# Optimization experiments

Hardware: AMD Instinct MI355X
Metric: run time of the kernel (lower is better)

Reference implementation:

```python
import jax, jax.numpy as jnp
import numpy as np

EPS = 1e-12

def l2norm(x, axis):
    # torch.nn.functional.normalize: x / max(||x||_2, eps)
    n = jnp.sqrt(jnp.sum(x * x, axis=axis, keepdims=True))
    return x / jnp.maximum(n, EPS)

def setup_inputs() -> dict:
    key = jax.random.key(0)
    k1, k2, k3, k4 = jax.random.split(key, 4)
    B, Cf, H, W = 128, 1024, 16, 16
    n_att, dv = 312, 300
    img = jax.random.normal(k1, (B, Cf, H, W), dtype=jnp.float32)
    # V is initialized from row-normalized w2v embeddings in the module
    V = l2norm(jax.random.normal(k2, (n_att, dv), dtype=jnp.float32), axis=1)
    W1 = jax.random.normal(k3, (dv, Cf), dtype=jnp.float32)
    W2 = jax.random.normal(k4, (dv, Cf), dtype=jnp.float32)
    return {"img": img, "V": V, "W1": W1, "W2": W2}

def reference(img, V, W1, W2):
    vv = l2norm(V, axis=1)                               # [i, v]
    B, Cf, H, Wd = img.shape
    av = l2norm(img.reshape(B, Cf, H * Wd), axis=1)      # [b, f, r]
    Q = vv @ W1                                          # [i, f]
    A = jnp.einsum('if,bfr->bir', Q, av)                 # attention logits
    A = jax.nn.softmax(A, axis=-1)
    F_p = jnp.einsum('bir,bfr->bif', A, av)              # attended features
    Pred_att = jnp.einsum('if,bif->bi', vv @ W2, F_p)
    return Pred_att
```

## Files before the change

kernel.cpp:

```cpp
#include <hip/hip_runtime.h>
#include <math.h>

#define NB   128
#define CF   1024
#define RR   256
#define NA   312
#define DV   300
#define MT   640
#define NKC  32
#define NQ   160
#define NPI  320
#define ABYTES 40960

typedef _Float16 half8  __attribute__((ext_vector_type(8)));
typedef _Float16 half4  __attribute__((ext_vector_type(4)));
typedef float float16v  __attribute__((ext_vector_type(16)));
typedef float float4v   __attribute__((ext_vector_type(4)));

__device__ __forceinline__ void gll16(const void* g, void* l) {
    __builtin_amdgcn_global_load_lds(
        (const __attribute__((address_space(1))) void*)g,
        (__attribute__((address_space(3))) void*)l, 16, 0, 0);
}

__launch_bounds__(256, 4)
__global__ void k_q(const float* __restrict__ V, const float* __restrict__ W1,
                    const float* __restrict__ W2, _Float16* __restrict__ Qb) {
    int ib = blockIdx.x;
    int t  = threadIdx.x;
    bool isQ2 = ib >= 80;
    int i0l = (ib - (isQ2 ? 80 : 0)) * 4;
    __shared__ float inv4[4];
    float acc[4][4];
    #pragma unroll
    for (int ii = 0; ii < 4; ++ii)
        #pragma unroll
        for (int j = 0; j < 4; ++j) acc[ii][j] = 0.f;
    if (i0l < NA) {
        int row = t >> 6, l64 = t & 63;
        float s = 0.f;
        for (int v = l64; v < DV; v += 64) { float x = V[(i0l + row) * DV + v]; s += x * x; }
        #pragma unroll
        for (int o = 32; o; o >>= 1) s += __shfl_xor(s, o, 64);
        if (l64 == 0) inv4[row] = 1.f / fmaxf(sqrtf(s), 1e-12f);
        __syncthreads();
        const float* W  = isQ2 ? W2 : W1;
        const float* Vb = V + (size_t)i0l * DV;
        for (int v = 0; v < DV; v += 2) {
            float4v w0 = *(const float4v*)(W + (size_t)v * CF + t * 4);
            float4v w1 = *(const float4v*)(W + (size_t)(v + 1) * CF + t * 4);
            #pragma unroll
            for (int ii = 0; ii < 4; ++ii) {
                float a0 = Vb[(size_t)ii * DV + v];
                float a1 = Vb[(size_t)ii * DV + v + 1];
                #pragma unroll
                for (int j = 0; j < 4; ++j) acc[ii][j] += a0 * w0[j] + a1 * w1[j];
            }
        }
        #pragma unroll
        for (int ii = 0; ii < 4; ++ii)
            #pragma unroll
            for (int j = 0; j < 4; ++j) acc[ii][j] *= inv4[ii];
    }
    int fg = t >> 3;
    int fo = (t & 7) * 4;
    int q12 = isQ2 ? 1 : 0;
    #pragma unroll
    for (int ii = 0; ii < 4; ++ii) {
        half4 h;
        #pragma unroll
        for (int j = 0; j < 4; ++j) h[j] = (_Float16)acc[ii][j];
        *(half4*)&Qb[((size_t)fg * MT + (2 * (i0l + ii) + q12)) * 32 + fo] = h;
    }
}

extern __shared__ char smem[];
__launch_bounds__(512, 2)
__global__ void k_fused(const float* __restrict__ img, const _Float16* __restrict__ Qb,
                        float* __restrict__ pm, float* __restrict__ ps,
                        float* __restrict__ pd) {
    int lin = blockIdx.x;
    int b   = lin >> 1;
    int rh  = lin & 1;

    int tid  = threadIdx.x;
    int lane = tid & 63;
    int w    = tid >> 6;
    int wm   = w >> 1;
    int wn   = w & 1;
    int nl   = lane & 31;
    int kh   = lane >> 5;

    int aG[5];
    #pragma unroll
    for (int j = 0; j < 5; ++j) {
        int s = tid + j * 512;
        aG[j] = ((s % 640) * 4 + (s / 640)) * 16;
    }
    const char* gA = (const char*)Qb;

    int c_lo = wn * 64 + nl;
    const float* pB = img + (size_t)b * CF * RR + (size_t)rh * 128 + c_lo
                      + (size_t)kh * 8 * RR;

    float16v acc[5][2];
    #pragma unroll
    for (int i = 0; i < 5; ++i)
        #pragma unroll
        for (int j = 0; j < 2; ++j)
            #pragma unroll
            for (int gi = 0; gi < 16; ++gi) acc[i][j][gi] = 0.f;
    float ssq0 = 0.f, ssq1 = 0.f;
    float Bv0[2][8], Bv1[2][8];
    half8 bf0[2], bf1[2];

    #define AGLL(kc_, bsel) do {                                                   \
        int kcl = (kc_) < NKC ? (kc_) : (NKC - 1);                                 \
        const char* aS = gA + (size_t)kcl * ABYTES;                                \
        char* buf_ = smem + (size_t)(bsel) * ABYTES;                               \
        _Pragma("unroll")                                                          \
        for (int j = 0; j < 5; ++j) gll16(aS + aG[j], buf_ + (tid + j * 512) * 16); \
    } while (0)

    #define BLOAD(kc_) do {                                                        \
        int kcl = (kc_) < NKC ? (kc_) : (NKC - 1);                                 \
        const float* p = pB + (size_t)kcl * 32 * RR;                               \
        _Pragma("unroll")                                                          \
        for (int ks = 0; ks < 2; ++ks)                                             \
            _Pragma("unroll")                                                      \
            for (int j = 0; j < 8; ++j) {                                          \
                Bv0[ks][j] = p[(size_t)(ks * 16 + j) * RR];                        \
                Bv1[ks][j] = p[(size_t)(ks * 16 + j) * RR + 32];                   \
            }                                                                      \
    } while (0)

    #define BCVT() do {                                                            \
        _Pragma("unroll")                                                          \
        for (int ks = 0; ks < 2; ++ks)                                             \
            _Pragma("unroll")                                                      \
            for (int j = 0; j < 8; ++j) {                                          \
                float x0 = Bv0[ks][j], x1 = Bv1[ks][j];                            \
                ssq0 += x0 * x0; ssq1 += x1 * x1;                                  \
                bf0[ks][j] = (_Float16)x0; bf1[ks][j] = (_Float16)x1;              \
            }                                                                      \
    } while (0)

    #define COMPUTE(bsel) do {                                                     \
        const char* Al = smem + (size_t)(bsel) * ABYTES;                           \
        _Pragma("unroll")                                                          \
        for (int ks = 0; ks < 2; ++ks) {                                           \
            int kb = ks * 2 + kh;                                                  \
            _Pragma("unroll")                                                      \
            for (int mt = 0; mt < 5; ++mt) {                                       \
                half8 af = *(const half8*)(Al + ((size_t)kb * 640 + wm * 160 + mt * 32 + nl) * 16); \
                acc[mt][0] = __builtin_amdgcn_mfma_f32_32x32x16_f16(af, bf0[ks], acc[mt][0], 0, 0, 0); \
                acc[mt][1] = __builtin_amdgcn_mfma_f32_32x32x16_f16(af, bf1[ks], acc[mt][1], 0, 0, 0); \
            }                                                                      \
        }                                                                          \
    } while (0)

    AGLL(0, 0);
    BLOAD(0);
    asm volatile("s_waitcnt vmcnt(32)" ::: "memory");
    __builtin_amdgcn_s_barrier();
    AGLL(1, 1);
    __builtin_amdgcn_sched_barrier(0);

    #pragma unroll 1
    for (int kc = 0; kc < NKC; ++kc) {
        asm volatile("s_waitcnt vmcnt(5)" ::: "memory");
        BCVT();
        BLOAD(kc + 1);
        __builtin_amdgcn_sched_barrier(0);
        __builtin_amdgcn_s_setprio(1);
        COMPUTE(kc & 1);
        __builtin_amdgcn_s_setprio(0);
        __builtin_amdgcn_sched_barrier(0);
        asm volatile("s_waitcnt vmcnt(32)" ::: "memory");
        __builtin_amdgcn_s_barrier();
        AGLL(kc + 2, kc & 1);
        __builtin_amdgcn_sched_barrier(0);
    }
    asm volatile("s_waitcnt vmcnt(0) lgkmcnt(0)" ::: "memory");
    __builtin_amdgcn_s_barrier();
    __builtin_amdgcn_sched_barrier(0);
    #undef AGLL
    #undef BLOAD
    #undef BCVT
    #undef COMPUTE

    float* mred = (float*)smem;
    float* mg   = (float*)(smem + 2560);
    float* sred = (float*)(smem + 3840);
    float* dred = (float*)(smem + 6400);

    ssq0 += __shfl_xor(ssq0, 32, 64);
    ssq1 += __shfl_xor(ssq1, 32, 64);
    float iv0 = 1.f / fmaxf(sqrtf(ssq0), 1e-12f);
    float iv1 = 1.f / fmaxf(sqrtf(ssq1), 1e-12f);
    #pragma unroll
    for (int mt = 0; mt < 5; ++mt)
        #pragma unroll
        for (int gi = 0; gi < 16; ++gi) {
            acc[mt][0][gi] *= iv0;
            acc[mt][1][gi] *= iv1;
        }

    #pragma unroll
    for (int mt = 0; mt < 5; ++mt) {
        #pragma unroll
        for (int e = 0; e < 8; ++e) {
            int g = 2 * e;
            float mx = fmaxf(acc[mt][0][g], acc[mt][1][g]);
            #pragma unroll
            for (int off = 1; off <= 16; off <<= 1)
                mx = fmaxf(mx, __shfl_xor(mx, off, 64));
            if (nl == 0) {
                int row = (g & 3) + 8 * (g >> 2) + 4 * kh;
                mred[wn * NPI + wm * 80 + mt * 16 + (row >> 1)] = mx;
            }
        }
    }
    __syncthreads();
    if (tid < NPI) mg[tid] = fmaxf(mred[tid], mred[NPI + tid]);
    __syncthreads();

    #pragma unroll
    for (int mt = 0; mt < 5; ++mt) {
        #pragma unroll
        for (int e = 0; e < 8; ++e) {
            int g = 2 * e;
            int row = (g & 3) + 8 * (g >> 2) + 4 * kh;
            int i   = wm * 80 + mt * 16 + (row >> 1);
            float m  = mg[i];
            float e0 = __expf(acc[mt][0][g] - m);
            float e1 = __expf(acc[mt][1][g] - m);
            float s = e0 + e1;
            float d = e0 * acc[mt][0][g + 1] + e1 * acc[mt][1][g + 1];
            #pragma unroll
            for (int off = 1; off <= 16; off <<= 1) {
                s += __shfl_xor(s, off, 64);
                d += __shfl_xor(d, off, 64);
            }
            if (nl == 0) {
                sred[wn * NPI + i] = s;
                dred[wn * NPI + i] = d;
            }
        }
    }
    __syncthreads();
    if (tid < NPI) {
        size_t pb = ((size_t)b * 2 + rh) * NPI + tid;
        pm[pb] = mg[tid];
        ps[pb] = sred[tid] + sred[NPI + tid];
        pd[pb] = dred[tid] + dred[NPI + tid];
    }
}

__launch_bounds__(256, 4)
__global__ void k_comb(const float* __restrict__ pm, const float* __restrict__ ps,
                       const float* __restrict__ pd, float* __restrict__ out) {
    int idx = blockIdx.x * 256 + threadIdx.x;
    int b = idx / NPI;
    int i = idx - b * NPI;
    float m0 = pm[(size_t)(b * 2) * NPI + i];
    float m1 = pm[(size_t)(b * 2 + 1) * NPI + i];
    float m  = fmaxf(m0, m1);
    float w0 = __expf(m0 - m), w1 = __expf(m1 - m);
    float s = ps[(size_t)(b * 2) * NPI + i] * w0 + ps[(size_t)(b * 2 + 1) * NPI + i] * w1;
    float d = pd[(size_t)(b * 2) * NPI + i] * w0 + pd[(size_t)(b * 2 + 1) * NPI + i] * w1;
    if (i < NA) out[(size_t)b * NA + i] = d / s;
}

extern "C" void kernel_launch(void* const* d_in, const int* in_sizes, int n_in,
                              void* d_out, int out_size, void* d_ws, size_t ws_size,
                              hipStream_t stream) {
    const float* img = (const float*)d_in[0];
    const float* V   = (const float*)d_in[1];
    const float* W1  = (const float*)d_in[2];
    const float* W2  = (const float*)d_in[3];
    float* out = (float*)d_out;

    char* ws = (char*)d_ws;
    size_t off = 0;
    _Float16* Qb = (_Float16*)(ws + off); off += (size_t)NKC * MT * 32 * 2;
    float*    pm = (float*)(ws + off);    off += (size_t)NB * 2 * NPI * 4;
    float*    ps = (float*)(ws + off);    off += (size_t)NB * 2 * NPI * 4;
    float*    pd = (float*)(ws + off);    off += (size_t)NB * 2 * NPI * 4;

    static bool attr_done = false;
    if (!attr_done) {
        (void)hipFuncSetAttribute((const void*)k_fused,
                                  hipFuncAttributeMaxDynamicSharedMemorySize, 2 * ABYTES);
        attr_done = true;
    }

    k_q<<<dim3(NQ), 256, 0, stream>>>(V, W1, W2, Qb);
    k_fused<<<dim3(256), 512, 2 * ABYTES, stream>>>(img, Qb, pm, ps, pd);
    k_comb<<<dim3(160), 256, 0, stream>>>(pm, ps, pd, out);
}
```

Before: 273.4 us.

## Split fused attention kernel across M quarters into smaller 128-thread blocks

The fused kernel now launches 1024 blocks of two waves, each covering one quarter of the attribute rows for a batch/r-half, instead of 256 blocks of eight waves. The Q tile staged in LDS shrinks to that quarter and moves to static shared memory, so the dynamic-LDS attribute setup is dropped. This aims to spread work over more CUs and raise occupancy. In exchange, each image slice is read and converted four times, relying on L2 for reuse.

After: 278.1 us. Within noise of the previous version (+1.7%).

```diff
diff --git a/kernel.cpp b/kernel.cpp
--- a/kernel.cpp
+++ b/kernel.cpp
@@ -10,7 +10,8 @@
 #define NKC  32
 #define NQ   160
 #define NPI  320
-#define ABYTES 40960
+#define ACHUNK 40960
+#define ATILE  12288
 
 typedef _Float16 half8  __attribute__((ext_vector_type(8)));
 typedef _Float16 half4  __attribute__((ext_vector_type(4)));
@@ -74,28 +75,32 @@
     }
 }
 
-extern __shared__ char smem[];
-__launch_bounds__(512, 2)
+__launch_bounds__(128, 2)
 __global__ void k_fused(const float* __restrict__ img, const _Float16* __restrict__ Qb,
                         float* __restrict__ pm, float* __restrict__ ps,
                         float* __restrict__ pd) {
+    __shared__ __align__(16) char smem_s[2 * ATILE];
+
     int lin = blockIdx.x;
-    int b   = lin >> 1;
-    int rh  = lin & 1;
+    int b   = lin & 127;
+    int sub = lin >> 7;
+    int rh  = sub >> 2;
+    int mq  = sub & 3;
 
     int tid  = threadIdx.x;
     int lane = tid & 63;
-    int w    = tid >> 6;
-    int wm   = w >> 1;
-    int wn   = w & 1;
+    int wn   = tid >> 6;
     int nl   = lane & 31;
     int kh   = lane >> 5;
 
-    int aG[5];
-    #pragma unroll
-    for (int j = 0; j < 5; ++j) {
-        int s = tid + j * 512;
-        aG[j] = ((s % 640) * 4 + (s / 640)) * 16;
+    int aG[6];
+    #pragma unroll
+    for (int j = 0; j < 6; ++j) {
+        int s  = tid + j * 128;
+        int kb = s / 192;
+        int r  = s % 192;
+        int rc = r < 160 ? r : 159;
+        aG[j] = (mq * 160 + rc) * 64 + kb * 16;
     }
     const char* gA = (const char*)Qb;
 
@@ -116,10 +121,10 @@
 
     #define AGLL(kc_, bsel) do {                                                   \
         int kcl = (kc_) < NKC ? (kc_) : (NKC - 1);                                 \
-        const char* aS = gA + (size_t)kcl * ABYTES;                                \
-        char* buf_ = smem + (size_t)(bsel) * ABYTES;                               \
-        _Pragma("unroll")                                                          \
-        for (int j = 0; j < 5; ++j) gll16(aS + aG[j], buf_ + (tid + j * 512) * 16); \
+        const char* aS = gA + (size_t)kcl * ACHUNK;                                \
+        char* buf_ = smem_s + (int)(bsel) * ATILE;                                 \
+        _Pragma("unroll")                                                          \
+        for (int j = 0; j < 6; ++j) gll16(aS + aG[j], buf_ + (tid + j * 128) * 16); \
     } while (0)
 
     #define BLOAD(kc_) do {                                                        \
@@ -146,13 +151,13 @@
     } while (0)
 
     #define COMPUTE(bsel) do {                                                     \
-        const char* Al = smem + (size_t)(bsel) * ABYTES;                           \
+        const char* Al = smem_s + (int)(bsel) * ATILE;                             \
         _Pragma("unroll")                                                          \
         for (int ks = 0; ks < 2; ++ks) {                                           \
             int kb = ks * 2 + kh;                                                  \
             _Pragma("unroll")                                                      \
             for (int mt = 0; mt < 5; ++mt) {                                       \
-                half8 af = *(const half8*)(Al + ((size_t)kb * 640 + wm * 160 + mt * 32 + nl) * 16); \
+                half8 af = *(const half8*)(Al + (kb * 192 + mt * 32 + nl) * 16);   \
                 acc[mt][0] = __builtin_amdgcn_mfma_f32_32x32x16_f16(af, bf0[ks], acc[mt][0], 0, 0, 0); \
                 acc[mt][1] = __builtin_amdgcn_mfma_f32_32x32x16_f16(af, bf1[ks], acc[mt][1], 0, 0, 0); \
             }                                                                      \
@@ -168,7 +173,7 @@
 
     #pragma unroll 1
     for (int kc = 0; kc < NKC; ++kc) {
-        asm volatile("s_waitcnt vmcnt(5)" ::: "memory");
+        asm volatile("s_waitcnt vmcnt(6)" ::: "memory");
         BCVT();
         BLOAD(kc + 1);
         __builtin_amdgcn_sched_barrier(0);
@@ -189,10 +194,10 @@
     #undef BCVT
     #undef COMPUTE
 
-    float* mred = (float*)smem;
-    float* mg   = (float*)(smem + 2560);
-    float* sred = (float*)(smem + 3840);
-    float* dred = (float*)(smem + 6400);
+    float* mred = (float*)smem_s;
+    float* mg   = (float*)(smem_s + 1024);
+    float* sred = (float*)(smem_s + 1536);
+    float* dred = (float*)(smem_s + 2560);
 
     ssq0 += __shfl_xor(ssq0, 32, 64);
     ssq1 += __shfl_xor(ssq1, 32, 64);
@@ -217,12 +222,12 @@
                 mx = fmaxf(mx, __shfl_xor(mx, off, 64));
             if (nl == 0) {
                 int row = (g & 3) + 8 * (g >> 2) + 4 * kh;
-                mred[wn * NPI + wm * 80 + mt * 16 + (row >> 1)] = mx;
+                mred[wn * 80 + mt * 16 + (row >> 1)] = mx;
             }
         }
     }
     __syncthreads();
-    if (tid < NPI) mg[tid] = fmaxf(mred[tid], mred[NPI + tid]);
+    if (tid < 80) mg[tid] = fmaxf(mred[tid], mred[80 + tid]);
     __syncthreads();
 
     #pragma unroll
@@ -231,7 +236,7 @@
         for (int e = 0; e < 8; ++e) {
             int g = 2 * e;
             int row = (g & 3) + 8 * (g >> 2) + 4 * kh;
-            int i   = wm * 80 + mt * 16 + (row >> 1);
+            int i   = mt * 16 + (row >> 1);
             float m  = mg[i];
             float e0 = __expf(acc[mt][0][g] - m);
             float e1 = __expf(acc[mt][1][g] - m);
@@ -243,17 +248,17 @@
                 d += __shfl_xor(d, off, 64);
             }
             if (nl == 0) {
-                sred[wn * NPI + i] = s;
-                dred[wn * NPI + i] = d;
+                sred[wn * 80 + i] = s;
+                dred[wn * 80 + i] = d;
             }
         }
     }
     __syncthreads();
-    if (tid < NPI) {
-        size_t pb = ((size_t)b * 2 + rh) * NPI + tid;
+    if (tid < 80) {
+        size_t pb = ((size_t)b * 2 + rh) * NPI + mq * 80 + tid;
         pm[pb] = mg[tid];
-        ps[pb] = sred[tid] + sred[NPI + tid];
-        pd[pb] = dred[tid] + dred[NPI + tid];
+        ps[pb] = sred[tid] + sred[80 + tid];
+        pd[pb] = dred[tid] + dred[80 + tid];
     }
 }
 
@@ -288,14 +293,7 @@
     float*    ps = (float*)(ws + off);    off += (size_t)NB * 2 * NPI * 4;
     float*    pd = (float*)(ws + off);    off += (size_t)NB * 2 * NPI * 4;
 
-    static bool attr_done = false;
-    if (!attr_done) {
-        (void)hipFuncSetAttribute((const void*)k_fused,
-                                  hipFuncAttributeMaxDynamicSharedMemorySize, 2 * ABYTES);
-        attr_done = true;
-    }
-
     k_q<<<dim3(NQ), 256, 0, stream>>>(V, W1, W2, Qb);
-    k_fused<<<dim3(256), 512, 2 * ABYTES, stream>>>(img, Qb, pm, ps, pd);
+    k_fused<<<dim3(1024), 128, 0, stream>>>(img, Qb, pm, ps, pd);
     k_comb<<<dim3(160), 256, 0, stream>>>(pm, ps, pd, out);
 }
```

## Split fused kernel over M halves and stage B tile through LDS

Applied to the files above, without the earlier changes.

Each block now handles half of the 640 query rows, which doubles the grid to 512 blocks of 256 threads. Image columns are loaded as coalesced float2, converted to fp16 and written into an LDS B tile, so every wave no longer issues strided scalar loads for its own B fragments. The column sum of squares is reduced across waves through LDS, and the main loop is unrolled by two with register double-buffering of the B loads. In exchange, each image element is now read twice (once per M half), and there are extra LDS writes and barriers per k-chunk.

New measurement: 276.2 us. About the same (+1.0%).

```diff
diff --git a/kernel.cpp b/kernel.cpp
--- a/kernel.cpp
+++ b/kernel.cpp
@@ -10,12 +10,16 @@
 #define NKC  32
 #define NQ   160
 #define NPI  320
-#define ABYTES 40960
+#define ACHUNK 40960
+#define ATILE  20480
+#define BTILE  8192
+#define BUFSZ  28672
 
 typedef _Float16 half8  __attribute__((ext_vector_type(8)));
 typedef _Float16 half4  __attribute__((ext_vector_type(4)));
 typedef float float16v  __attribute__((ext_vector_type(16)));
 typedef float float4v   __attribute__((ext_vector_type(4)));
+typedef float float2v   __attribute__((ext_vector_type(2)));
 
 __device__ __forceinline__ void gll16(const void* g, void* l) {
     __builtin_amdgcn_global_load_lds(
@@ -74,14 +78,17 @@
     }
 }
 
-extern __shared__ char smem[];
-__launch_bounds__(512, 2)
+__launch_bounds__(256, 2)
 __global__ void k_fused(const float* __restrict__ img, const _Float16* __restrict__ Qb,
                         float* __restrict__ pm, float* __restrict__ ps,
                         float* __restrict__ pd) {
+    __shared__ __align__(16) char smem_s[2 * BUFSZ];
+
     int lin = blockIdx.x;
-    int b   = lin >> 1;
-    int rh  = lin & 1;
+    int b   = lin & 127;
+    int sub = lin >> 7;
+    int rh  = sub & 1;
+    int mh  = sub >> 1;
 
     int tid  = threadIdx.x;
     int lane = tid & 63;
@@ -94,14 +101,15 @@
     int aG[5];
     #pragma unroll
     for (int j = 0; j < 5; ++j) {
-        int s = tid + j * 512;
-        aG[j] = ((s % 640) * 4 + (s / 640)) * 16;
+        int s  = tid + j * 256;
+        int kb = s / 320;
+        int r  = s % 320;
+        aG[j] = ((mh * 320 + r) * 4 + kb) * 16;
     }
     const char* gA = (const char*)Qb;
 
-    int c_lo = wn * 64 + nl;
-    const float* pB = img + (size_t)b * CF * RR + (size_t)rh * 128 + c_lo
-                      + (size_t)kh * 8 * RR;
+    const float* gB = img + (size_t)b * CF * RR + (size_t)w * 8 * RR
+                      + (size_t)rh * 128 + 2 * lane;
 
     float16v acc[5][2];
     #pragma unroll
@@ -110,94 +118,121 @@
         for (int j = 0; j < 2; ++j)
             #pragma unroll
             for (int gi = 0; gi < 16; ++gi) acc[i][j][gi] = 0.f;
-    float ssq0 = 0.f, ssq1 = 0.f;
-    float Bv0[2][8], Bv1[2][8];
-    half8 bf0[2], bf1[2];
+    float ssq_e = 0.f, ssq_o = 0.f;
+    float2v R0[8], R1[8];
 
     #define AGLL(kc_, bsel) do {                                                   \
         int kcl = (kc_) < NKC ? (kc_) : (NKC - 1);                                 \
-        const char* aS = gA + (size_t)kcl * ABYTES;                                \
-        char* buf_ = smem + (size_t)(bsel) * ABYTES;                               \
+        const char* aS = gA + (size_t)kcl * ACHUNK;                                \
+        char* buf_ = smem_s + (int)(bsel) * BUFSZ;                                 \
         _Pragma("unroll")                                                          \
-        for (int j = 0; j < 5; ++j) gll16(aS + aG[j], buf_ + (tid + j * 512) * 16); \
-    } while (0)
-
-    #define BLOAD(kc_) do {                                                        \
+        for (int j = 0; j < 5; ++j) gll16(aS + aG[j], buf_ + (tid + j * 256) * 16); \
+    } while (0)
+
+    #define BLOAD(kc_, R) do {                                                     \
         int kcl = (kc_) < NKC ? (kc_) : (NKC - 1);                                 \
-        const float* p = pB + (size_t)kcl * 32 * RR;                               \
+        const float* p = gB + (size_t)kcl * 32 * RR;                               \
         _Pragma("unroll")                                                          \
-        for (int ks = 0; ks < 2; ++ks)                                             \
-            _Pragma("unroll")                                                      \
-            for (int j = 0; j < 8; ++j) {                                          \
-                Bv0[ks][j] = p[(size_t)(ks * 16 + j) * RR];                        \
-                Bv1[ks][j] = p[(size_t)(ks * 16 + j) * RR + 32];                   \
-            }                                                                      \
-    } while (0)
-
-    #define BCVT() do {                                                            \
+        for (int j = 0; j < 8; ++j) (R)[j] = *(const float2v*)(p + (size_t)j * RR); \
+    } while (0)
+
+    #define CVTW(R, bsel) do {                                                     \
+        half8 he, ho;                                                              \
         _Pragma("unroll")                                                          \
-        for (int ks = 0; ks < 2; ++ks)                                             \
-            _Pragma("unroll")                                                      \
-            for (int j = 0; j < 8; ++j) {                                          \
-                float x0 = Bv0[ks][j], x1 = Bv1[ks][j];                            \
-                ssq0 += x0 * x0; ssq1 += x1 * x1;                                  \
-                bf0[ks][j] = (_Float16)x0; bf1[ks][j] = (_Float16)x1;              \
-            }                                                                      \
+        for (int j = 0; j < 8; ++j) {                                              \
+            float xe = (R)[j][0], xo = (R)[j][1];                                  \
+            ssq_e += xe * xe; ssq_o += xo * xo;                                    \
+            he[j] = (_Float16)xe; ho[j] = (_Float16)xo;                            \
+        }                                                                          \
+        char* bb = smem_s + (int)(bsel) * BUFSZ + ATILE + w * 2048 + lane * 32;    \
+        *(half8*)bb = he;                                                          \
+        *(half8*)(bb + 16) = ho;                                                   \
     } while (0)
 
     #define COMPUTE(bsel) do {                                                     \
-        const char* Al = smem + (size_t)(bsel) * ABYTES;                           \
+        const char* Al = smem_s + (int)(bsel) * BUFSZ;                             \
+        const char* Bl = Al + ATILE;                                               \
         _Pragma("unroll")                                                          \
         for (int ks = 0; ks < 2; ++ks) {                                           \
             int kb = ks * 2 + kh;                                                  \
+            half8 bf0 = *(const half8*)(Bl + (kb * 128 + wn * 64 + nl) * 16);      \
+            half8 bf1 = *(const half8*)(Bl + (kb * 128 + wn * 64 + 32 + nl) * 16); \
             _Pragma("unroll")                                                      \
             for (int mt = 0; mt < 5; ++mt) {                                       \
-                half8 af = *(const half8*)(Al + ((size_t)kb * 640 + wm * 160 + mt * 32 + nl) * 16); \
-                acc[mt][0] = __builtin_amdgcn_mfma_f32_32x32x16_f16(af, bf0[ks], acc[mt][0], 0, 0, 0); \
-                acc[mt][1] = __builtin_amdgcn_mfma_f32_32x32x16_f16(af, bf1[ks], acc[mt][1], 0, 0, 0); \
+                half8 af = *(const half8*)(Al + (kb * 320 + wm * 160 + mt * 32 + nl) * 16); \
+                acc[mt][0] = __builtin_amdgcn_mfma_f32_32x32x16_f16(af, bf0, acc[mt][0], 0, 0, 0); \
+                acc[mt][1] = __builtin_amdgcn_mfma_f32_32x32x16_f16(af, bf1, acc[mt][1], 0, 0, 0); \
             }                                                                      \
         }                                                                          \
     } while (0)
 
+    BLOAD(0, R0);
     AGLL(0, 0);
-    BLOAD(0);
-    asm volatile("s_waitcnt vmcnt(32)" ::: "memory");
+    BLOAD(1, R1);
+    asm volatile("s_waitcnt vmcnt(13)" ::: "memory");
+    CVTW(R0, 0);
+    asm volatile("s_waitcnt vmcnt(8)" ::: "memory");
+    asm volatile("s_waitcnt lgkmcnt(0)" ::: "memory");
     __builtin_amdgcn_s_barrier();
     AGLL(1, 1);
     __builtin_amdgcn_sched_barrier(0);
 
+    #define ITER(kc_, Rcur, Rnxt) do {                                             \
+        BLOAD((kc_) + 2, Rnxt);                         \
+        asm volatile("s_waitcnt vmcnt(13)" ::: "memory");         \
+        CVTW(Rcur, ((kc_) + 1) & 1);                     \
+        __builtin_amdgcn_sched_barrier(0);                                         \
+        __builtin_amdgcn_s_setprio(1);                                             \
+        COMPUTE((kc_) & 1);                                                        \
+        __builtin_amdgcn_s_setprio(0);                                             \
+        __builtin_amdgcn_sched_barrier(0);                                         \
+        asm volatile("s_waitcnt vmcnt(8)" ::: "memory");       \
+        asm volatile("s_waitcnt lgkmcnt(0)" ::: "memory");                         \
+        __builtin_amdgcn_s_barrier();                      \
+        AGLL((kc_) + 2, (kc_) & 1);                       \
+        __builtin_amdgcn_sched_barrier(0);                                         \
+    } while (0)
+
     #pragma unroll 1
-    for (int kc = 0; kc < NKC; ++kc) {
-        asm volatile("s_waitcnt vmcnt(5)" ::: "memory");
-        BCVT();
-        BLOAD(kc + 1);
-        __builtin_amdgcn_sched_barrier(0);
-        __builtin_amdgcn_s_setprio(1);
-        COMPUTE(kc & 1);
-        __builtin_amdgcn_s_setprio(0);
-        __builtin_amdgcn_sched_barrier(0);
-        asm volatile("s_waitcnt vmcnt(32)" ::: "memory");
-        __builtin_amdgcn_s_barrier();
-        AGLL(kc + 2, kc & 1);
-        __builtin_amdgcn_sched_barrier(0);
-    }
+    for (int kc = 0; kc < NKC - 2; kc += 2) {
+        ITER(kc,     R1, R0);
+        ITER(kc + 1, R0, R1);
+    }
+    ITER(NKC - 2, R1, R0);
+    __builtin_amdgcn_s_setprio(1);
+    COMPUTE((NKC - 1) & 1);
+    __builtin_amdgcn_s_setprio(0);
     asm volatile("s_waitcnt vmcnt(0) lgkmcnt(0)" ::: "memory");
     __builtin_amdgcn_s_barrier();
     __builtin_amdgcn_sched_barrier(0);
+    #undef ITER
     #undef AGLL
     #undef BLOAD
-    #undef BCVT
+    #undef CVTW
     #undef COMPUTE
 
-    float* mred = (float*)smem;
-    float* mg   = (float*)(smem + 2560);
-    float* sred = (float*)(smem + 3840);
-    float* dred = (float*)(smem + 6400);
-
-    ssq0 += __shfl_xor(ssq0, 32, 64);
-    ssq1 += __shfl_xor(ssq1, 32, 64);
-    float iv0 = 1.f / fmaxf(sqrtf(ssq0), 1e-12f);
-    float iv1 = 1.f / fmaxf(sqrtf(ssq1), 1e-12f);
+    float* ssq_lds = (float*)smem_s;
+    float* ssq_r   = (float*)(smem_s + 2048);
+    float* mred    = (float*)(smem_s + 2560);
+    float* mg      = (float*)(smem_s + 3840);
+    float* sred    = (float*)(smem_s + 4480);
+    float* dred    = (float*)(smem_s + 5760);
+
+    ssq_lds[(w * 64 + lane) * 2 + 0] = ssq_e;
+    ssq_lds[(w * 64 + lane) * 2 + 1] = ssq_o;
+    __syncthreads();
+    if (tid < 128) {
+        int rp = tid >> 1, par = tid & 1;
+        float sv = 0.f;
+        #pragma unroll
+        for (int o = 0; o < 4; ++o) sv += ssq_lds[((o * 64 + rp) * 2) + par];
+        ssq_r[tid] = sv;
+    }
+    __syncthreads();
+    int c0 = wn * 64 + nl;
+    float iv0 = 1.f / fmaxf(sqrtf(ssq_r[c0]), 1e-12f);
+    float iv1 = 1.f / fmaxf(sqrtf(ssq_r[c0 + 32]), 1e-12f);
+    __syncthreads();
     #pragma unroll
     for (int mt = 0; mt < 5; ++mt)
         #pragma unroll
@@ -217,12 +252,12 @@
                 mx = fmaxf(mx, __shfl_xor(mx, off, 64));
             if (nl == 0) {
                 int row = (g & 3) + 8 * (g >> 2) + 4 * kh;
-                mred[wn * NPI + wm * 80 + mt * 16 + (row >> 1)] = mx;
+                mred[wn * 160 + wm * 80 + mt * 16 + (row >> 1)] = mx;
             }
         }
     }
     __syncthreads();
-    if (tid < NPI) mg[tid] = fmaxf(mred[tid], mred[NPI + tid]);
+    if (tid < 160) mg[tid] = fmaxf(mred[tid], mred[160 + tid]);
     __syncthreads();
 
     #pragma unroll
@@ -243,17 +278,17 @@
                 d += __shfl_xor(d, off, 64);
             }
             if (nl == 0) {
-                sred[wn * NPI + i] = s;
-                dred[wn * NPI + i] = d;
+                sred[wn * 160 + i] = s;
+                dred[wn * 160 + i] = d;
             }
         }
     }
     __syncthreads();
-    if (tid < NPI) {
-        size_t pb = ((size_t)b * 2 + rh) * NPI + tid;
+    if (tid < 160) {
+        size_t pb = ((size_t)b * 2 + rh) * NPI + mh * 160 + tid;
         pm[pb] = mg[tid];
-        ps[pb] = sred[tid] + sred[NPI + tid];
-        pd[pb] = dred[tid] + dred[NPI + tid];
+        ps[pb] = sred[tid] + sred[160 + tid];
+        pd[pb] = dred[tid] + dred[160 + tid];
     }
 }
 
@@ -288,14 +323,7 @@
     float*    ps = (float*)(ws + off);    off += (size_t)NB * 2 * NPI * 4;
     float*    pd = (float*)(ws + off);    off += (size_t)NB * 2 * NPI * 4;
 
-    static bool attr_done = false;
-    if (!attr_done) {
-        (void)hipFuncSetAttribute((const void*)k_fused,
-                                  hipFuncAttributeMaxDynamicSharedMemorySize, 2 * ABYTES);
-        attr_done = true;
-    }
-
     k_q<<<dim3(NQ), 256, 0, stream>>>(V, W1, W2, Qb);
-    k_fused<<<dim3(256), 512, 2 * ABYTES, stream>>>(img, Qb, pm, ps, pd);
+    k_fused<<<dim3(512), 256, 0, stream>>>(img, Qb, pm, ps, pd);
     k_comb<<<dim3(160), 256, 0, stream>>>(pm, ps, pd, out);
 }
```

## Split fused kernel into smaller blocks loading Q directly into registers

Applied to the files above, without the earlier changes.

Replaces the 512-thread block, which staged Q tiles through LDS with async global-to-LDS loads and barriers, by 256-thread blocks that load Q fragments straight from global memory into registers. The grid grows from 256 to 1024 blocks by splitting each batch over four column quarters and two halves of the attention rows, and the combine kernel now merges four partial softmax states. This removes LDS staging and block barriers and raises parallelism. The cost is that Q is reread from global/L2 by many more blocks, with less reuse per block.

Result: slower. 451.6 us (+65.2%).

```diff
diff --git a/kernel.cpp b/kernel.cpp
--- a/kernel.cpp
+++ b/kernel.cpp
@@ -9,19 +9,12 @@
 #define MT   640
 #define NKC  32
 #define NQ   160
-#define NPI  320
-#define ABYTES 40960
+#define NPP  320
 
 typedef _Float16 half8  __attribute__((ext_vector_type(8)));
 typedef _Float16 half4  __attribute__((ext_vector_type(4)));
 typedef float float16v  __attribute__((ext_vector_type(16)));
 typedef float float4v   __attribute__((ext_vector_type(4)));
-
-__device__ __forceinline__ void gll16(const void* g, void* l) {
-    __builtin_amdgcn_global_load_lds(
-        (const __attribute__((address_space(1))) void*)g,
-        (__attribute__((address_space(3))) void*)l, 16, 0, 0);
-}
 
 __launch_bounds__(256, 4)
 __global__ void k_q(const float* __restrict__ V, const float* __restrict__ W1,
@@ -74,14 +67,15 @@
     }
 }
 
-extern __shared__ char smem[];
-__launch_bounds__(512, 2)
+__launch_bounds__(256, 3)
 __global__ void k_fused(const float* __restrict__ img, const _Float16* __restrict__ Qb,
                         float* __restrict__ pm, float* __restrict__ ps,
                         float* __restrict__ pd) {
     int lin = blockIdx.x;
-    int b   = lin >> 1;
-    int rh  = lin & 1;
+    int b   = lin & 127;
+    int sub = lin >> 7;
+    int rq  = sub & 3;
+    int mh  = sub >> 2;
 
     int tid  = threadIdx.x;
     int lane = tid & 63;
@@ -91,138 +85,106 @@
     int nl   = lane & 31;
     int kh   = lane >> 5;
 
-    int aG[5];
-    #pragma unroll
-    for (int j = 0; j < 5; ++j) {
-        int s = tid + j * 512;
-        aG[j] = ((s % 640) * 4 + (s / 640)) * 16;
-    }
-    const char* gA = (const char*)Qb;
-
-    int c_lo = wn * 64 + nl;
-    const float* pB = img + (size_t)b * CF * RR + (size_t)rh * 128 + c_lo
-                      + (size_t)kh * 8 * RR;
-
-    float16v acc[5][2];
+    const char* gA = (const char*)Qb + (size_t)(mh * 320 + wm * 160 + nl) * 64 + kh * 16;
+    const float* gB = img + (size_t)b * CF * RR + (size_t)kh * 8 * RR
+                      + rq * 64 + wn * 32 + nl;
+
+    float16v acc[5];
     #pragma unroll
     for (int i = 0; i < 5; ++i)
         #pragma unroll
-        for (int j = 0; j < 2; ++j)
-            #pragma unroll
-            for (int gi = 0; gi < 16; ++gi) acc[i][j][gi] = 0.f;
-    float ssq0 = 0.f, ssq1 = 0.f;
-    float Bv0[2][8], Bv1[2][8];
-    half8 bf0[2], bf1[2];
-
-    #define AGLL(kc_, bsel) do {                                                   \
-        int kcl = (kc_) < NKC ? (kc_) : (NKC - 1);                                 \
-        const char* aS = gA + (size_t)kcl * ABYTES;                                \
-        char* buf_ = smem + (size_t)(bsel) * ABYTES;                               \
-        _Pragma("unroll")                                                          \
-        for (int j = 0; j < 5; ++j) gll16(aS + aG[j], buf_ + (tid + j * 512) * 16); \
-    } while (0)
+        for (int gi = 0; gi < 16; ++gi) acc[i][gi] = 0.f;
+    float ssq = 0.f;
+    float Bv[16];
+    half8 bf0, bf1;
+    half8 Av[5][2];
 
     #define BLOAD(kc_) do {                                                        \
         int kcl = (kc_) < NKC ? (kc_) : (NKC - 1);                                 \
-        const float* p = pB + (size_t)kcl * 32 * RR;                               \
+        const float* p = gB + (size_t)kcl * 32 * RR;                               \
         _Pragma("unroll")                                                          \
         for (int ks = 0; ks < 2; ++ks)                                             \
             _Pragma("unroll")                                                      \
-            for (int j = 0; j < 8; ++j) {                                          \
-                Bv0[ks][j] = p[(size_t)(ks * 16 + j) * RR];                        \
-                Bv1[ks][j] = p[(size_t)(ks * 16 + j) * RR + 32];                   \
-            }                                                                      \
+            for (int j = 0; j < 8; ++j)                                            \
+                Bv[ks * 8 + j] = p[(size_t)(ks * 16 + j) * RR];                    \
+    } while (0)
+
+    #define ALOAD(kc_) do {                                                        \
+        int kcl = (kc_) < NKC ? (kc_) : (NKC - 1);                                 \
+        const char* a = gA + (size_t)kcl * (MT * 64);                              \
+        _Pragma("unroll")                                                          \
+        for (int mt = 0; mt < 5; ++mt)                                             \
+            _Pragma("unroll")                                                      \
+            for (int ks = 0; ks < 2; ++ks)                                         \
+                Av[mt][ks] = *(const half8*)(a + mt * 32 * 64 + ks * 32);          \
     } while (0)
 
     #define BCVT() do {                                                            \
         _Pragma("unroll")                                                          \
-        for (int ks = 0; ks < 2; ++ks)                                             \
-            _Pragma("unroll")                                                      \
-            for (int j = 0; j < 8; ++j) {                                          \
-                float x0 = Bv0[ks][j], x1 = Bv1[ks][j];                            \
-                ssq0 += x0 * x0; ssq1 += x1 * x1;                                  \
-                bf0[ks][j] = (_Float16)x0; bf1[ks][j] = (_Float16)x1;              \
-            }                                                                      \
-    } while (0)
-
-    #define COMPUTE(bsel) do {                                                     \
-        const char* Al = smem + (size_t)(bsel) * ABYTES;                           \
-        _Pragma("unroll")                                                          \
-        for (int ks = 0; ks < 2; ++ks) {                                           \
-            int kb = ks * 2 + kh;                                                  \
-            _Pragma("unroll")                                                      \
-            for (int mt = 0; mt < 5; ++mt) {                                       \
-                half8 af = *(const half8*)(Al + ((size_t)kb * 640 + wm * 160 + mt * 32 + nl) * 16); \
-                acc[mt][0] = __builtin_amdgcn_mfma_f32_32x32x16_f16(af, bf0[ks], acc[mt][0], 0, 0, 0); \
-                acc[mt][1] = __builtin_amdgcn_mfma_f32_32x32x16_f16(af, bf1[ks], acc[mt][1], 0, 0, 0); \
-            }                                                                      \
+        for (int j = 0; j < 8; ++j) {                                              \
+            float x0 = Bv[j], x1 = Bv[8 + j];                                      \
+            ssq += x0 * x0; ssq += x1 * x1;                                        \
+            bf0[j] = (_Float16)x0; bf1[j] = (_Float16)x1;                          \
         }                                                                          \
     } while (0)
 
-    AGLL(0, 0);
+    #define COMPUTE() do {                                                         \
+        _Pragma("unroll")                                                          \
+        for (int mt = 0; mt < 5; ++mt)                                             \
+            acc[mt] = __builtin_amdgcn_mfma_f32_32x32x16_f16(Av[mt][0], bf0, acc[mt], 0, 0, 0); \
+        _Pragma("unroll")                                                          \
+        for (int mt = 0; mt < 5; ++mt)                                             \
+            acc[mt] = __builtin_amdgcn_mfma_f32_32x32x16_f16(Av[mt][1], bf1, acc[mt], 0, 0, 0); \
+    } while (0)
+
     BLOAD(0);
-    asm volatile("s_waitcnt vmcnt(32)" ::: "memory");
-    __builtin_amdgcn_s_barrier();
-    AGLL(1, 1);
-    __builtin_amdgcn_sched_barrier(0);
-
+    ALOAD(0);
     #pragma unroll 1
     for (int kc = 0; kc < NKC; ++kc) {
-        asm volatile("s_waitcnt vmcnt(5)" ::: "memory");
+        __builtin_amdgcn_sched_barrier(0);
         BCVT();
         BLOAD(kc + 1);
         __builtin_amdgcn_sched_barrier(0);
         __builtin_amdgcn_s_setprio(1);
-        COMPUTE(kc & 1);
+        COMPUTE();
         __builtin_amdgcn_s_setprio(0);
         __builtin_amdgcn_sched_barrier(0);
-        asm volatile("s_waitcnt vmcnt(32)" ::: "memory");
-        __builtin_amdgcn_s_barrier();
-        AGLL(kc + 2, kc & 1);
-        __builtin_amdgcn_sched_barrier(0);
-    }
-    asm volatile("s_waitcnt vmcnt(0) lgkmcnt(0)" ::: "memory");
-    __builtin_amdgcn_s_barrier();
-    __builtin_amdgcn_sched_barrier(0);
-    #undef AGLL
+        ALOAD(kc + 1);
+    }
     #undef BLOAD
+    #undef ALOAD
     #undef BCVT
     #undef COMPUTE
 
-    float* mred = (float*)smem;
-    float* mg   = (float*)(smem + 2560);
-    float* sred = (float*)(smem + 3840);
-    float* dred = (float*)(smem + 6400);
-
-    ssq0 += __shfl_xor(ssq0, 32, 64);
-    ssq1 += __shfl_xor(ssq1, 32, 64);
-    float iv0 = 1.f / fmaxf(sqrtf(ssq0), 1e-12f);
-    float iv1 = 1.f / fmaxf(sqrtf(ssq1), 1e-12f);
+    __shared__ float mred[2][160];
+    __shared__ float mg[160];
+    __shared__ float sred[2][160];
+    __shared__ float dred[2][160];
+
+    ssq += __shfl_xor(ssq, 32, 64);
+    float iv = 1.f / fmaxf(sqrtf(ssq), 1e-12f);
     #pragma unroll
     for (int mt = 0; mt < 5; ++mt)
         #pragma unroll
-        for (int gi = 0; gi < 16; ++gi) {
-            acc[mt][0][gi] *= iv0;
-            acc[mt][1][gi] *= iv1;
-        }
+        for (int gi = 0; gi < 16; ++gi) acc[mt][gi] *= iv;
 
     #pragma unroll
     for (int mt = 0; mt < 5; ++mt) {
         #pragma unroll
         for (int e = 0; e < 8; ++e) {
             int g = 2 * e;
-            float mx = fmaxf(acc[mt][0][g], acc[mt][1][g]);
+            float mx = acc[mt][g];
             #pragma unroll
             for (int off = 1; off <= 16; off <<= 1)
                 mx = fmaxf(mx, __shfl_xor(mx, off, 64));
             if (nl == 0) {
                 int row = (g & 3) + 8 * (g >> 2) + 4 * kh;
-                mred[wn * NPI + wm * 80 + mt * 16 + (row >> 1)] = mx;
+                mred[wn][wm * 80 + mt * 16 + (row >> 1)] = mx;
             }
         }
     }
     __syncthreads();
-    if (tid < NPI) mg[tid] = fmaxf(mred[tid], mred[NPI + tid]);
+    if (tid < 160) mg[tid] = fmaxf(mred[0][tid], mred[1][tid]);
     __syncthreads();
 
     #pragma unroll
@@ -233,27 +195,26 @@
             int row = (g & 3) + 8 * (g >> 2) + 4 * kh;
             int i   = wm * 80 + mt * 16 + (row >> 1);
             float m  = mg[i];
-            float e0 = __expf(acc[mt][0][g] - m);
-            float e1 = __expf(acc[mt][1][g] - m);
-            float s = e0 + e1;
-            float d = e0 * acc[mt][0][g + 1] + e1 * acc[mt][1][g + 1];
+            float e0 = __expf(acc[mt][g] - m);
+            float s = e0;
+            float d = e0 * acc[mt][g + 1];
             #pragma unroll
             for (int off = 1; off <= 16; off <<= 1) {
                 s += __shfl_xor(s, off, 64);
                 d += __shfl_xor(d, off, 64);
             }
             if (nl == 0) {
-                sred[wn * NPI + i] = s;
-                dred[wn * NPI + i] = d;
+                sred[wn][i] = s;
+                dred[wn][i] = d;
             }
         }
     }
     __syncthreads();
-    if (tid < NPI) {
-        size_t pb = ((size_t)b * 2 + rh) * NPI + tid;
+    if (tid < 160) {
+        size_t pb = ((size_t)b * 4 + rq) * NPP + mh * 160 + tid;
         pm[pb] = mg[tid];
-        ps[pb] = sred[tid] + sred[NPI + tid];
-        pd[pb] = dred[tid] + dred[NPI + tid];
+        ps[pb] = sred[0][tid] + sred[1][tid];
+        pd[pb] = dred[0][tid] + dred[1][tid];
     }
 }
 
@@ -261,14 +222,15 @@
 __global__ void k_comb(const float* __restrict__ pm, const float* __restrict__ ps,
                        const float* __restrict__ pd, float* __restrict__ out) {
     int idx = blockIdx.x * 256 + threadIdx.x;
-    int b = idx / NPI;
-    int i = idx - b * NPI;
-    float m0 = pm[(size_t)(b * 2) * NPI + i];
-    float m1 = pm[(size_t)(b * 2 + 1) * NPI + i];
-    float m  = fmaxf(m0, m1);
+    int b = idx / NPP;
+    int i = idx - b * NPP;
+    size_t base = (size_t)b * 4 * NPP + i;
+    float m0 = pm[base], m1 = pm[base + NPP], m2 = pm[base + 2 * NPP], m3 = pm[base + 3 * NPP];
+    float m  = fmaxf(fmaxf(m0, m1), fmaxf(m2, m3));
     float w0 = __expf(m0 - m), w1 = __expf(m1 - m);
-    float s = ps[(size_t)(b * 2) * NPI + i] * w0 + ps[(size_t)(b * 2 + 1) * NPI + i] * w1;
-    float d = pd[(size_t)(b * 2) * NPI + i] * w0 + pd[(size_t)(b * 2 + 1) * NPI + i] * w1;
+    float w2 = __expf(m2 - m), w3 = __expf(m3 - m);
+    float s = ps[base] * w0 + ps[base + NPP] * w1 + ps[base + 2 * NPP] * w2 + ps[base + 3 * NPP] * w3;
+    float d = pd[base] * w0 + pd[base + NPP] * w1 + pd[base + 2 * NPP] * w2 + pd[base + 3 * NPP] * w3;
     if (i < NA) out[(size_t)b * NA + i] = d / s;
 }
 
@@ -284,18 +246,11 @@
     char* ws = (char*)d_ws;
     size_t off = 0;
     _Float16* Qb = (_Float16*)(ws + off); off += (size_t)NKC * MT * 32 * 2;
-    float*    pm = (float*)(ws + off);    off += (size_t)NB * 2 * NPI * 4;
-    float*    ps = (float*)(ws + off);    off += (size_t)NB * 2 * NPI * 4;
-    float*    pd = (float*)(ws + off);    off += (size_t)NB * 2 * NPI * 4;
-
-    static bool attr_done = false;
-    if (!attr_done) {
-        (void)hipFuncSetAttribute((const void*)k_fused,
-                                  hipFuncAttributeMaxDynamicSharedMemorySize, 2 * ABYTES);
-        attr_done = true;
-    }
+    float*    pm = (float*)(ws + off);    off += (size_t)NB * 4 * NPP * 4;
+    float*    ps = (float*)(ws + off);    off += (size_t)NB * 4 * NPP * 4;
+    float*    pd = (float*)(ws + off);    off += (size_t)NB * 4 * NPP * 4;
 
     k_q<<<dim3(NQ), 256, 0, stream>>>(V, W1, W2, Qb);
-    k_fused<<<dim3(256), 512, 2 * ABYTES, stream>>>(img, Qb, pm, ps, pd);
+    k_fused<<<dim3(1024), 256, 0, stream>>>(img, Qb, pm, ps, pd);
     k_comb<<<dim3(160), 256, 0, stream>>>(pm, ps, pd, out);
 }
```
